# Optimization experiments

Hardware: AMD Instinct MI355X
Metric: run time of the kernel (lower is better)

Reference implementation:

```python
import jax, jax.numpy as jnp
import numpy as np

B, L, D = 4, 4096, 1024
K = D // 4

def setup_inputs() -> dict:
    key = jax.random.key(0)
    ks = jax.random.split(key, 16)
    def w(k, sh):
        return jax.random.normal(k, sh, dtype=jnp.float32) * 0.02
    return {
        'x': jax.random.normal(ks[0], (B, L, D), dtype=jnp.float32),
        'Wk1': w(ks[1], (D, D)), 'bk1': jnp.zeros((D,), jnp.float32),
        'Wk2': w(ks[2], (D, K * 4)), 'bk2': jnp.zeros((K * 4,), jnp.float32),
        'Wq1': w(ks[3], (D, D)), 'bq1': jnp.zeros((D,), jnp.float32),
        'Wq2': w(ks[4], (D, K * 4)), 'bq2': jnp.zeros((K * 4,), jnp.float32),
        'Wv': w(ks[5], (D, D)), 'bv': jnp.zeros((D,), jnp.float32),
        'gamma': jnp.ones((D,), jnp.float32), 'beta': jnp.zeros((D,), jnp.float32),
        'Wo': w(ks[6], (D, D)), 'bo': jnp.zeros((D,), jnp.float32),
    }

def _normalize(q, eps=1e-12):
    n = jnp.sqrt(jnp.sum(q * q, axis=-1, keepdims=True))
    return q / jnp.maximum(n, eps)

def _quat_conj(q):
    return q * jnp.asarray([1., -1., -1., -1.], dtype=q.dtype)

def _quat_mul(q1, q2):
    w1, x1, y1, z1 = q1[..., 0], q1[..., 1], q1[..., 2], q1[..., 3]
    w2, x2, y2, z2 = q2[..., 0], q2[..., 1], q2[..., 2], q2[..., 3]
    w = w1 * w2 - x1 * x2 - y1 * y2 - z1 * z2
    x = w1 * x2 + x1 * w2 + y1 * z2 - z1 * y2
    y = w1 * y2 - x1 * z2 + y1 * w2 + z1 * x2
    z = w1 * z2 + x1 * y2 - y1 * x2 + z1 * w2
    return jnp.stack([w, x, y, z], axis=-1)

def _quat_rotate(q, v):
    return _quat_mul(_quat_mul(q, v), _quat_conj(q))

def _mlp(x, W1, b1, W2, b2):
    h = jax.nn.gelu(x @ W1 + b1, approximate=False)
    return h @ W2 + b2

def _layernorm(x, g, b, eps=1e-5):
    mu = jnp.mean(x, axis=-1, keepdims=True)
    var = jnp.var(x, axis=-1, keepdims=True)
    return (x - mu) * jax.lax.rsqrt(var + eps) * g + b

def reference(x, Wk1, bk1, Wk2, bk2, Wq1, bq1, Wq2, bq2, Wv, bv, gamma, beta, Wo, bo):
    b, l, d = x.shape
    k = d // 4
    key_q = _normalize(_mlp(x, Wk1, bk1, Wk2, bk2).reshape(b, l, k, 4))
    query_q = _normalize(_mlp(x, Wq1, bq1, Wq2, bq2).reshape(b, l, k, 4))
    value = (x @ Wv + bv).reshape(b, l, k, 4)
    rotated = _quat_rotate(key_q, value)            # [B,L,K,4]
    memory = jnp.cumsum(rotated, axis=1)            # prefix-sum memory
    retrieved = _quat_rotate(_quat_conj(query_q), memory).reshape(b, l, d)
    norm = jnp.sqrt(jnp.arange(1, l + 1, dtype=x.dtype)).reshape(1, l, 1)
    out = _layernorm(retrieved / norm, gamma, beta) @ Wo + bo
    return x + out
```

## Files before the change

kernel.cpp:

```cpp
#include <hip/hip_runtime.h>
#include <cstddef>
#include <cstdint>

static constexpr int Bb  = 4;
static constexpr int Ll  = 4096;
static constexpr int Mm  = 16384;
static constexpr int KK  = 1024;
static constexpr int NCH = 128;
static constexpr int CHL = 32;

typedef __attribute__((ext_vector_type(8))) short short8;
typedef __attribute__((ext_vector_type(4))) float f32x4;

#define AS1C(p) ((const __attribute__((address_space(1))) void*)(p))
#define AS3(p)  ((__attribute__((address_space(3))) void*)(p))

__device__ __forceinline__ float b2f(unsigned short u) {
    union { unsigned int i; float f; } c; c.i = ((unsigned int)u) << 16; return c.f;
}
__device__ __forceinline__ unsigned short f2b(float f) {
    union { float f; unsigned int i; } c; c.f = f;
    unsigned int r = c.i + 0x7fffu + ((c.i >> 16) & 1u);
    return (unsigned short)(r >> 16);
}
__device__ __forceinline__ float4 bq2f(ushort4 u) {
    return make_float4(b2f(u.x), b2f(u.y), b2f(u.z), b2f(u.w));
}
__device__ __forceinline__ ushort4 f2bq(float4 v) {
    ushort4 o; o.x = f2b(v.x); o.y = f2b(v.y); o.z = f2b(v.z); o.w = f2b(v.w); return o;
}
__device__ __forceinline__ float4 qmul(const float4 a, const float4 b) {
    float4 r;
    r.x = a.x * b.x - a.y * b.y - a.z * b.z - a.w * b.w;
    r.y = a.x * b.y + a.y * b.x + a.z * b.w - a.w * b.z;
    r.z = a.x * b.z - a.y * b.w + a.z * b.x + a.w * b.y;
    r.w = a.x * b.w + a.y * b.z - a.z * b.y + a.w * b.x;
    return r;
}
__device__ __forceinline__ float4 qconj(const float4 a) {
    return make_float4(a.x, -a.y, -a.z, -a.w);
}
__device__ __forceinline__ float4 qnorm(const float4 a) {
    float n = sqrtf(a.x * a.x + a.y * a.y + a.z * a.z + a.w * a.w);
    float inv = 1.0f / fmaxf(n, 1e-12f);
    return make_float4(a.x * inv, a.y * inv, a.z * inv, a.w * inv);
}
__device__ __forceinline__ float gelu_fast(float v) {
    const float a = fabsf(v) * 0.70710678118654752f;
    const float t = 1.0f / (1.0f + 0.3275911f * a);
    const float p = t * (0.254829592f + t * (-0.284496736f + t * (1.421413741f
                   + t * (-1.453152027f + t * 1.061405429f))));
    const float e = __expf(-a * a);
    const float erfa = 1.0f - p * e;
    return 0.5f * v * (1.0f + copysignf(erfa, v));
}

__global__ __launch_bounds__(256)
void conv_k(const float* __restrict__ src, unsigned short* __restrict__ dst, int n4)
{
    const int i = blockIdx.x * 256 + threadIdx.x;
    if (i >= n4) return;
    const float4 v = reinterpret_cast<const float4*>(src)[i];
    reinterpret_cast<ushort4*>(dst)[i] = f2bq(v);
}

__global__ __launch_bounds__(256)
void wtrans_k(const float* __restrict__ src, unsigned short* __restrict__ dst)
{
    __shared__ float t[32][33];
    const int tx = threadIdx.x, ty = threadIdx.y;
    const int n0 = blockIdx.x * 32, k0 = blockIdx.y * 32;
    #pragma unroll
    for (int j = ty; j < 32; j += 8)
        t[j][tx] = src[(size_t)(k0 + j) * 1024 + n0 + tx];
    __syncthreads();
    #pragma unroll
    for (int j = ty; j < 32; j += 8)
        dst[(size_t)(n0 + j) * 1024 + k0 + tx] = f2b(t[tx][j]);
}

__global__ __launch_bounds__(256)
void bcat_k(const float* __restrict__ bk1, const float* __restrict__ bq1,
            const float* __restrict__ bv,  const float* __restrict__ bk2,
            const float* __restrict__ bq2, float* __restrict__ b1,
            float* __restrict__ b2)
{
    const int i = blockIdx.x * 256 + threadIdx.x;
    if (i < 3072) b1[i] = (i < 1024) ? bk1[i] : (i < 2048 ? bq1[i - 1024] : bv[i - 2048]);
    if (i < 2048) b2[i] = (i < 1024) ? bk2[i] : bq2[i - 1024];
}

template<int MODE>
__global__ __launch_bounds__(256, 3)
void gemm128_k(const unsigned short* __restrict__ A, int astride,
               const unsigned short* __restrict__ BT,
               const float* __restrict__ bias,
               const float* __restrict__ resid,
               unsigned short* __restrict__ outH,
               unsigned short* __restrict__ outV,
               float* __restrict__ outF,
               int Nn)
{
    __shared__ char smem[49152];
    const int tid  = threadIdx.x;
    const int lane = tid & 63;
    const int w    = tid >> 6;
    const int wr   = w >> 1;
    const int wc   = w & 1;

    const int nwg = gridDim.x;
    const int cpx = nwg >> 3;
    const int bid = blockIdx.x;
    const int swz = (bid & 7) * cpx + (bid >> 3);
    const int nTN = Nn >> 7;
    const int m0  = (swz / nTN) << 7;
    const int n0  = (swz % nTN) << 7;
    const int aoff = (MODE == 1 && n0 >= 1024) ? 1024 : 0;

    const unsigned short* gA[2];
    const unsigned short* gB[2];
    #pragma unroll
    for (int c2 = 0; c2 < 2; ++c2) {
        const int s = c2 * 256 + tid;
        const int line = s >> 3;
        const int u = (s & 7) ^ (line & 7);
        const int r = 2 * line + (u >> 2);
        const int kcs = u & 3;
        gA[c2] = A + (size_t)(m0 + r) * astride + aoff + kcs * 8;
        gB[c2] = BT + (size_t)(n0 + r) * KK + kcs * 8;
    }

    auto STAGE = [&](int c, int koff) {
        #pragma unroll
        for (int c2 = 0; c2 < 2; ++c2)
            __builtin_amdgcn_global_load_lds(AS1C(gA[c2] + koff),
                AS3(smem + c * 16384 + c2 * 4096 + w * 1024), 16, 0, 0);
        #pragma unroll
        for (int c2 = 0; c2 < 2; ++c2)
            __builtin_amdgcn_global_load_lds(AS1C(gB[c2] + koff),
                AS3(smem + c * 16384 + 8192 + c2 * 4096 + w * 1024), 16, 0, 0);
    };

    const int kc4 = lane >> 4;
    const int rl  = lane & 15;
    int offA[4], offB[4];
    #pragma unroll
    for (int mi = 0; mi < 4; ++mi) {
        const int r = wr * 64 + mi * 16 + rl;
        offA[mi] = (r >> 1) * 128 + (((((r & 1) << 2) | kc4) ^ ((r >> 1) & 7)) << 4);
    }
    #pragma unroll
    for (int ni = 0; ni < 4; ++ni) {
        const int r = wc * 64 + ni * 16 + rl;
        offB[ni] = 8192 + (r >> 1) * 128 + (((((r & 1) << 2) | kc4) ^ ((r >> 1) & 7)) << 4);
    }

    f32x4 acc[4][4] = {};

    auto ITER = [&](int rb, int sb, int ks, int vm) {
        const int cb = rb * 16384;
        short8 af[4], bf[4];
        #pragma unroll
        for (int mi = 0; mi < 4; ++mi) af[mi] = *(const short8*)(smem + cb + offA[mi]);
        #pragma unroll
        for (int ni = 0; ni < 4; ++ni) bf[ni] = *(const short8*)(smem + cb + offB[ni]);
        if (ks >= 0) STAGE(sb, ks);
        #pragma unroll
        for (int mi = 0; mi < 4; ++mi)
            #pragma unroll
            for (int ni = 0; ni < 4; ++ni)
                acc[mi][ni] = __builtin_amdgcn_mfma_f32_16x16x32_bf16(af[mi], bf[ni], acc[mi][ni], 0, 0, 0);
        if (vm == 4)      asm volatile("s_waitcnt vmcnt(4)" ::: "memory");
        else if (vm == 0) asm volatile("s_waitcnt vmcnt(0)" ::: "memory");
        if (vm >= 0) __builtin_amdgcn_s_barrier();
    };

    STAGE(0, 0);
    STAGE(1, 32);
    asm volatile("s_waitcnt vmcnt(4)" ::: "memory");
    __builtin_amdgcn_s_barrier();

    #pragma unroll 1
    for (int t0 = 0; t0 < 30; t0 += 3) {
        ITER(0, 2, (t0 + 2) * 32, 4);
        ITER(1, 0, (t0 + 3) * 32, 4);
        ITER(2, 1, (t0 + 4) * 32, 4);
    }
    ITER(0, 0, -1, 0);
    ITER(1, 0, -1, -1);
    __syncthreads();

    const int colb = n0 + wc * 64 + rl;
    float bv[4];
    #pragma unroll
    for (int ni = 0; ni < 4; ++ni) bv[ni] = bias[colb + ni * 16];

    if (MODE == 2) {
        const int rowb = m0 + wr * 64 + kc4 * 4;
        #pragma unroll
        for (int ni = 0; ni < 4; ++ni) {
            const int col = colb + ni * 16;
            #pragma unroll
            for (int mi = 0; mi < 4; ++mi) {
                #pragma unroll
                for (int rr = 0; rr < 4; ++rr) {
                    const int row = rowb + mi * 16 + rr;
                    const size_t ix = (size_t)row * 1024 + col;
                    outF[ix] = acc[mi][ni][rr] + bv[ni] + resid[ix];
                }
            }
        }
    } else {
        const bool dogelu = (MODE == 0) && (n0 < 2048);
        unsigned short* dst;
        int stride, col0;
        if (MODE == 0 && n0 >= 2048) { dst = outV; stride = 1024; col0 = n0 - 2048; }
        else                         { dst = outH; stride = 2048; col0 = n0; }
        unsigned short* eb = (unsigned short*)smem;
        #pragma unroll
        for (int pass = 0; pass < 2; ++pass) {
            if (wr == pass) {
                #pragma unroll
                for (int ni = 0; ni < 4; ++ni) {
                    const int col = wc * 64 + ni * 16 + rl;
                    #pragma unroll
                    for (int mi = 0; mi < 4; ++mi) {
                        #pragma unroll
                        for (int rr = 0; rr < 4; ++rr) {
                            float v = acc[mi][ni][rr] + bv[ni];
                            if (dogelu) v = gelu_fast(v);
                            eb[(mi * 16 + kc4 * 4 + rr) * 136 + col] = f2b(v);
                        }
                    }
                }
            }
            __syncthreads();
            const int row = tid >> 2;
            const int cc  = (tid & 3) * 32;
            const size_t grow = (size_t)(m0 + pass * 64 + row) * stride + col0 + cc;
            #pragma unroll
            for (int j = 0; j < 4; ++j)
                *(uint4*)(dst + grow + j * 8) = *(const uint4*)(eb + row * 136 + cc + j * 8);
            __syncthreads();
        }
    }
}

__global__ __launch_bounds__(256)
void rotfuse_k(const unsigned short* __restrict__ qb2, unsigned short* __restrict__ valb,
               float* __restrict__ part)
{
    const int idx = blockIdx.x * 256 + threadIdx.x;
    const int kq  = idx & 255;
    const int ch  = (idx >> 8) & 127;
    const int b   = idx >> 15;
    const int row0 = b * Ll + ch * CHL;
    float4 s = make_float4(0.f, 0.f, 0.f, 0.f);
    for (int i = 0; i < CHL; ++i) {
        const int row = row0 + i;
        const float4 q = qnorm(bq2f(*reinterpret_cast<const ushort4*>(qb2 + (size_t)row * 2048 + kq * 4)));
        ushort4* vp = reinterpret_cast<ushort4*>(valb + (size_t)row * 1024 + kq * 4);
        const float4 r = qmul(qmul(q, bq2f(*vp)), qconj(q));
        *vp = f2bq(r);
        s.x += r.x; s.y += r.y; s.z += r.z; s.w += r.w;
    }
    *reinterpret_cast<float4*>(part + (size_t)idx * 4) = s;
}

__global__ __launch_bounds__(256)
void scan2_k(float* __restrict__ part)
{
    const int idx = blockIdx.x * 256 + threadIdx.x;
    const int kq = idx & 255, b = idx >> 8;
    float4 run = make_float4(0.f, 0.f, 0.f, 0.f);
    for (int c = 0; c < NCH; ++c) {
        float4* p = reinterpret_cast<float4*>(part + (((size_t)(b * NCH + c)) * 256 + kq) * 4);
        const float4 t = *p;
        *p = run;
        run.x += t.x; run.y += t.y; run.z += t.z; run.w += t.w;
    }
}

__global__ __launch_bounds__(256)
void scan3ln_k(const unsigned short* __restrict__ rotb, const float* __restrict__ part,
               const unsigned short* __restrict__ qb2,
               const float* __restrict__ gamma, const float* __restrict__ beta,
               unsigned short* __restrict__ ln)
{
    const int kq = threadIdx.x;
    const int ch = blockIdx.x & (NCH - 1);
    const int b  = blockIdx.x >> 7;
    const int row0 = b * Ll + ch * CHL;
    float4 run = *reinterpret_cast<const float4*>(part + (((size_t)(b * NCH + ch)) * 256 + kq) * 4);

    __shared__ float red[2][2][4];
    const int wid = kq >> 6, lane = kq & 63;
    const float4 g4 = *reinterpret_cast<const float4*>(gamma + kq * 4);
    const float4 b4 = *reinterpret_cast<const float4*>(beta  + kq * 4);

    for (int i = 0; i < CHL; ++i) {
        const int row = row0 + i;
        const float4 v = bq2f(*reinterpret_cast<const ushort4*>(rotb + (size_t)row * 1024 + kq * 4));
        run.x += v.x; run.y += v.y; run.z += v.z; run.w += v.w;

        const float4 q = qnorm(bq2f(*reinterpret_cast<const ushort4*>(qb2 + (size_t)row * 2048 + 1024 + kq * 4)));
        float4 r = qmul(qmul(qconj(q), run), q);
        const float inv = rsqrtf((float)(ch * CHL + i + 1));
        r.x *= inv; r.y *= inv; r.z *= inv; r.w *= inv;

        float s  = r.x + r.y + r.z + r.w;
        float ss = r.x * r.x + r.y * r.y + r.z * r.z + r.w * r.w;
        #pragma unroll
        for (int off = 32; off > 0; off >>= 1) {
            s  += __shfl_xor(s, off);
            ss += __shfl_xor(ss, off);
        }
        if (lane == 0) { red[i & 1][0][wid] = s; red[i & 1][1][wid] = ss; }
        __syncthreads();
        const float sum = red[i & 1][0][0] + red[i & 1][0][1] + red[i & 1][0][2] + red[i & 1][0][3];
        const float ssq = red[i & 1][1][0] + red[i & 1][1][1] + red[i & 1][1][2] + red[i & 1][1][3];
        const float mu  = sum * (1.0f / 1024.0f);
        const float var = ssq * (1.0f / 1024.0f) - mu * mu;
        const float sc  = rsqrtf(var + 1e-5f);

        float4 o;
        o.x = (r.x - mu) * sc * g4.x + b4.x;
        o.y = (r.y - mu) * sc * g4.y + b4.y;
        o.z = (r.z - mu) * sc * g4.z + b4.z;
        o.w = (r.w - mu) * sc * g4.w + b4.w;
        *reinterpret_cast<ushort4*>(ln + (size_t)row * 1024 + kq * 4) = f2bq(o);
    }
}

extern "C" void kernel_launch(void* const* d_in, const int* in_sizes, int n_in,
                              void* d_out, int out_size, void* d_ws, size_t ws_size,
                              hipStream_t stream)
{
    const float* x     = (const float*)d_in[0];
    const float* Wk1   = (const float*)d_in[1];
    const float* bk1   = (const float*)d_in[2];
    const float* Wk2   = (const float*)d_in[3];
    const float* bk2   = (const float*)d_in[4];
    const float* Wq1   = (const float*)d_in[5];
    const float* bq1   = (const float*)d_in[6];
    const float* Wq2   = (const float*)d_in[7];
    const float* bq2   = (const float*)d_in[8];
    const float* Wv    = (const float*)d_in[9];
    const float* bv    = (const float*)d_in[10];
    const float* gamma = (const float*)d_in[11];
    const float* beta  = (const float*)d_in[12];
    const float* Wo    = (const float*)d_in[13];
    const float* bo    = (const float*)d_in[14];
    float* out = (float*)d_out;

    const size_t TD = (size_t)Mm * 1024;
    const size_t DD = (size_t)1024 * 1024;

    unsigned short* qb2   = (unsigned short*)d_ws;
    unsigned short* xb    = qb2;
    unsigned short* wcat1 = qb2 + TD;
    unsigned short* h     = qb2 + 2 * TD;
    unsigned short* valb  = h + 2 * TD;
    unsigned short* wcat2 = valb + TD;
    unsigned short* woT   = wcat2 + 2 * DD;
    float*          bcat1 = (float*)(woT + DD);
    float*          bcat2 = bcat1 + 3072;
    float*          part  = bcat2 + 2048;

    const dim3 blk(256);
    const dim3 tblk(32, 8);
    const dim3 tgrid(32, 32);

    conv_k<<<(int)(TD / 4 / 256), blk, 0, stream>>>(x, xb, (int)(TD / 4));
    wtrans_k<<<tgrid, tblk, 0, stream>>>(Wk1, wcat1);
    wtrans_k<<<tgrid, tblk, 0, stream>>>(Wq1, wcat1 + DD);
    wtrans_k<<<tgrid, tblk, 0, stream>>>(Wv,  wcat1 + 2 * DD);
    wtrans_k<<<tgrid, tblk, 0, stream>>>(Wk2, wcat2);
    wtrans_k<<<tgrid, tblk, 0, stream>>>(Wq2, wcat2 + DD);
    wtrans_k<<<tgrid, tblk, 0, stream>>>(Wo,  woT);
    bcat_k<<<12, blk, 0, stream>>>(bk1, bq1, bv, bk2, bq2, bcat1, bcat2);

    gemm128_k<0><<<128 * 24, blk, 0, stream>>>(xb, 1024, wcat1, bcat1, nullptr, h, valb, nullptr, 3072);
    gemm128_k<1><<<128 * 16, blk, 0, stream>>>(h, 2048, wcat2, bcat2, nullptr, qb2, nullptr, nullptr, 2048);

    rotfuse_k<<<(Bb * NCH * 256) / 256, blk, 0, stream>>>(qb2, valb, part);
    scan2_k<<<4, blk, 0, stream>>>(part);
    scan3ln_k<<<Bb * NCH, blk, 0, stream>>>(valb, part, qb2, gamma, beta, h);

    gemm128_k<2><<<128 * 8, blk, 0, stream>>>(h, 1024, woT, bo, x, nullptr, nullptr, out, 1024);
}
```

Baseline: 437.6 us.

## Switch GEMM inner loop to 32x32x16 bf16 MFMA with matching LDS layout

Replaces the 4x4 grid of 16x16x32 MFMAs per wave with a 2x2 grid of 32x32x16 MFMAs over two k-substeps. The global-to-LDS staging swizzle, fragment offsets and epilogue row mapping are rewritten for the 32-row fragment layout. The aim is fewer LDS fragment reads per FLOP and higher MFMA throughput from the larger instruction. It risks new LDS bank conflicts from the changed swizzle and different register pressure.

```diff
diff --git a/kernel.cpp b/kernel.cpp
--- a/kernel.cpp
+++ b/kernel.cpp
@@ -9,8 +9,9 @@
 static constexpr int NCH = 128;
 static constexpr int CHL = 32;
 
-typedef __attribute__((ext_vector_type(8))) short short8;
-typedef __attribute__((ext_vector_type(4))) float f32x4;
+typedef __attribute__((ext_vector_type(8)))  short short8;
+typedef __attribute__((ext_vector_type(4)))  float f32x4;
+typedef __attribute__((ext_vector_type(16))) float f32x16;
 
 #define AS1C(p) ((const __attribute__((address_space(1))) void*)(p))
 #define AS3(p)  ((__attribute__((address_space(3))) void*)(p))
@@ -121,13 +122,15 @@
     const unsigned short* gB[2];
     #pragma unroll
     for (int c2 = 0; c2 < 2; ++c2) {
-        const int s = c2 * 256 + tid;
-        const int line = s >> 3;
-        const int u = (s & 7) ^ (line & 7);
-        const int r = 2 * line + (u >> 2);
-        const int kcs = u & 3;
-        gA[c2] = A + (size_t)(m0 + r) * astride + aoff + kcs * 8;
-        gB[c2] = BT + (size_t)(n0 + r) * KK + kcs * 8;
+        const int s_lin = c2 * 256 + tid;
+        const int line  = s_lin >> 3;
+        const int lu    = line & 31;
+        const int unit  = line >> 5;
+        const int v     = (s_lin & 7) ^ (lu & 7);
+        const int r     = lu * 4 + (v >> 1);
+        const int ke    = unit * 16 + (v & 1) * 8;
+        gA[c2] = A + (size_t)(m0 + r) * astride + aoff + ke;
+        gB[c2] = BT + (size_t)(n0 + r) * KK + ke;
     }
 
     auto STAGE = [&](int c, int koff) {
@@ -141,35 +144,44 @@
                 AS3(smem + c * 16384 + 8192 + c2 * 4096 + w * 1024), 16, 0, 0);
     };
 
-    const int kc4 = lane >> 4;
-    const int rl  = lane & 15;
-    int offA[4], offB[4];
+    const int l31 = lane & 31;
+    const int chk = lane >> 5;
+    int offA[2][2], offB[2][2];
     #pragma unroll
-    for (int mi = 0; mi < 4; ++mi) {
-        const int r = wr * 64 + mi * 16 + rl;
-        offA[mi] = (r >> 1) * 128 + (((((r & 1) << 2) | kc4) ^ ((r >> 1) & 7)) << 4);
-    }
-    #pragma unroll
-    for (int ni = 0; ni < 4; ++ni) {
-        const int r = wc * 64 + ni * 16 + rl;
-        offB[ni] = 8192 + (r >> 1) * 128 + (((((r & 1) << 2) | kc4) ^ ((r >> 1) & 7)) << 4);
-    }
-
-    f32x4 acc[4][4] = {};
-
-    auto ITER = [&](int rb, int sb, int ks, int vm) {
+    for (int ks = 0; ks < 2; ++ks) {
+        #pragma unroll
+        for (int mi = 0; mi < 2; ++mi) {
+            const int r = wr * 64 + mi * 32 + l31;
+            offA[ks][mi] = ks * 4096 + (r >> 2) * 128 + (((((r & 3) << 1) | chk) ^ ((r >> 2) & 7)) << 4);
+        }
+        #pragma unroll
+        for (int ni = 0; ni < 2; ++ni) {
+            const int r = wc * 64 + ni * 32 + l31;
+            offB[ks][ni] = 8192 + ks * 4096 + (r >> 2) * 128 + (((((r & 3) << 1) | chk) ^ ((r >> 2) & 7)) << 4);
+        }
+    }
+
+    f32x16 acc[2][2] = {};
+
+    auto ITER = [&](int rb, int sb, int ks2, int vm) {
         const int cb = rb * 16384;
-        short8 af[4], bf[4];
-        #pragma unroll
-        for (int mi = 0; mi < 4; ++mi) af[mi] = *(const short8*)(smem + cb + offA[mi]);
-        #pragma unroll
-        for (int ni = 0; ni < 4; ++ni) bf[ni] = *(const short8*)(smem + cb + offB[ni]);
-        if (ks >= 0) STAGE(sb, ks);
-        #pragma unroll
-        for (int mi = 0; mi < 4; ++mi)
+        short8 af[2][2], bf[2][2];
+        #pragma unroll
+        for (int ks = 0; ks < 2; ++ks) {
             #pragma unroll
-            for (int ni = 0; ni < 4; ++ni)
-                acc[mi][ni] = __builtin_amdgcn_mfma_f32_16x16x32_bf16(af[mi], bf[ni], acc[mi][ni], 0, 0, 0);
+            for (int mi = 0; mi < 2; ++mi) af[ks][mi] = *(const short8*)(smem + cb + offA[ks][mi]);
+            #pragma unroll
+            for (int ni = 0; ni < 2; ++ni) bf[ks][ni] = *(const short8*)(smem + cb + offB[ks][ni]);
+        }
+        if (ks2 >= 0) STAGE(sb, ks2);
+        #pragma unroll
+        for (int ks = 0; ks < 2; ++ks)
+            #pragma unroll
+            for (int mi = 0; mi < 2; ++mi)
+                #pragma unroll
+                for (int ni = 0; ni < 2; ++ni)
+                    acc[mi][ni] = __builtin_amdgcn_mfma_f32_32x32x16_bf16(
+                        af[ks][mi], bf[ks][ni], acc[mi][ni], 0, 0, 0);
         if (vm == 4)      asm volatile("s_waitcnt vmcnt(4)" ::: "memory");
         else if (vm == 0) asm volatile("s_waitcnt vmcnt(0)" ::: "memory");
         if (vm >= 0) __builtin_amdgcn_s_barrier();
@@ -190,23 +202,22 @@
     ITER(1, 0, -1, -1);
     __syncthreads();
 
-    const int colb = n0 + wc * 64 + rl;
-    float bv[4];
+    const int colb = n0 + wc * 64 + l31;
+    float bv[2];
     #pragma unroll
-    for (int ni = 0; ni < 4; ++ni) bv[ni] = bias[colb + ni * 16];
+    for (int ni = 0; ni < 2; ++ni) bv[ni] = bias[colb + ni * 32];
 
     if (MODE == 2) {
-        const int rowb = m0 + wr * 64 + kc4 * 4;
-        #pragma unroll
-        for (int ni = 0; ni < 4; ++ni) {
-            const int col = colb + ni * 16;
+        #pragma unroll
+        for (int ni = 0; ni < 2; ++ni) {
+            const int col = colb + ni * 32;
             #pragma unroll
-            for (int mi = 0; mi < 4; ++mi) {
+            for (int mi = 0; mi < 2; ++mi) {
                 #pragma unroll
-                for (int rr = 0; rr < 4; ++rr) {
-                    const int row = rowb + mi * 16 + rr;
+                for (int rg = 0; rg < 16; ++rg) {
+                    const int row = m0 + wr * 64 + mi * 32 + (rg & 3) + 8 * (rg >> 2) + 4 * chk;
                     const size_t ix = (size_t)row * 1024 + col;
-                    outF[ix] = acc[mi][ni][rr] + bv[ni] + resid[ix];
+                    outF[ix] = acc[mi][ni][rg] + bv[ni] + resid[ix];
                 }
             }
         }
@@ -221,15 +232,16 @@
         for (int pass = 0; pass < 2; ++pass) {
             if (wr == pass) {
                 #pragma unroll
-                for (int ni = 0; ni < 4; ++ni) {
-                    const int col = wc * 64 + ni * 16 + rl;
+                for (int ni = 0; ni < 2; ++ni) {
+                    const int col = wc * 64 + ni * 32 + l31;
                     #pragma unroll
-                    for (int mi = 0; mi < 4; ++mi) {
+                    for (int mi = 0; mi < 2; ++mi) {
                         #pragma unroll
-                        for (int rr = 0; rr < 4; ++rr) {
-                            float v = acc[mi][ni][rr] + bv[ni];
+                        for (int rg = 0; rg < 16; ++rg) {
+                            float v = acc[mi][ni][rg] + bv[ni];
                             if (dogelu) v = gelu_fast(v);
-                            eb[(mi * 16 + kc4 * 4 + rr) * 136 + col] = f2b(v);
+                            const int er2 = mi * 32 + (rg & 3) + 8 * (rg >> 2) + 4 * chk;
+                            eb[er2 * 136 + col] = f2b(v);
                         }
                     }
                 }
```

Result: slower. 474.0 us (+8.3%).
